# Kernel optimization log

Measured on AMD Instinct MI355X. Metric: run time of the kernel, lower is better.

The kernel has to match this reference:

```python
import jax, jax.numpy as jnp
import numpy as np

N = 100000
NFEAT = 128
NHID = 128
NCLASS = 40
E = 1600000
EPS = 1e-5


def _spmm(vals, src, dst, x, n):
    # y[dst] += vals * x[src]  (sparse adj @ x)
    return jax.ops.segment_sum(vals[:, None] * x[src], dst, num_segments=n)


def _bn(h, gamma, beta, rmean, rvar):
    # BatchNorm1d in eval mode (running statistics)
    return (h - rmean) * jax.lax.rsqrt(rvar + EPS) * gamma + beta


def setup_inputs() -> dict:
    key = jax.random.key(0)
    ks = jax.random.split(key, 24)
    inp = {
        'x': jax.random.normal(ks[0], (N, NFEAT), dtype=jnp.float32),
        'M': jax.random.uniform(ks[1], (N, 1), dtype=jnp.float32),
        'AM': jax.random.uniform(ks[2], (N, 1), dtype=jnp.float32),
        'srcZ': jax.random.randint(ks[3], (E,), 0, N, dtype=jnp.int32),
        'dstZ': jax.random.randint(ks[4], (E,), 0, N, dtype=jnp.int32),
        'valsZ': jax.random.uniform(ks[5], (E,), dtype=jnp.float32),
        'src': jax.random.randint(ks[6], (E,), 0, N, dtype=jnp.int32),
        'dst': jax.random.randint(ks[7], (E,), 0, N, dtype=jnp.int32),
        'vals': jax.random.uniform(ks[8], (E,), dtype=jnp.float32),
        # layer 0 (PaGConv) params
        'W0': jax.random.normal(ks[9], (NHID, NFEAT), dtype=jnp.float32) * (1.414 / np.sqrt(NFEAT)),
        'b0': jnp.zeros((NHID,), dtype=jnp.float32),
        'g0': jnp.ones((NHID,), dtype=jnp.float32),
        'be0': jnp.zeros((NHID,), dtype=jnp.float32),
        'rm0': jax.random.normal(ks[10], (NHID,), dtype=jnp.float32) * 0.1,
        'rv0': jax.random.uniform(ks[11], (NHID,), dtype=jnp.float32) + 0.5,
        # layer 1 (GConv) params
        'W1': jax.random.normal(ks[12], (NHID, NHID), dtype=jnp.float32) * (1.414 / np.sqrt(NHID)),
        'b1': jnp.zeros((NHID,), dtype=jnp.float32),
        'g1': jnp.ones((NHID,), dtype=jnp.float32),
        'be1': jnp.zeros((NHID,), dtype=jnp.float32),
        'rm1': jax.random.normal(ks[13], (NHID,), dtype=jnp.float32) * 0.1,
        'rv1': jax.random.uniform(ks[14], (NHID,), dtype=jnp.float32) + 0.5,
        # layer 2 (GConv) params
        'W2': jax.random.normal(ks[15], (NCLASS, NHID), dtype=jnp.float32) * (1.414 / np.sqrt(NHID)),
        'b2': jnp.zeros((NCLASS,), dtype=jnp.float32),
    }
    return inp


def reference(x, M, AM, srcZ, dstZ, valsZ, src, dst, vals,
              W0, b0, g0, be0, rm0, rv0,
              W1, b1, g1, be1, rm1, rv1,
              W2, b2):
    n = x.shape[0]
    # layer 0: PaGConv with adjZ: fc(spmm(adjZ, M*x) * AM), then BN + ReLU (dropout off in eval)
    h = _spmm(valsZ, srcZ, dstZ, M * x, n) * AM
    h = h @ W0.T + b0
    h = jax.nn.relu(_bn(h, g0, be0, rm0, rv0))
    # layer 1: GConv with adj: fc(spmm(adj, h)), then BN + ReLU
    h = _spmm(vals, src, dst, h, n)
    h = h @ W1.T + b1
    h = jax.nn.relu(_bn(h, g1, be1, rm1, rv1))
    # layer 2: GConv, then log_softmax
    h = _spmm(vals, src, dst, h, n)
    h = h @ W2.T + b2
    return jax.nn.log_softmax(h, axis=-1)
```

## Files before the change

kernel.cpp:

```cpp
#include <hip/hip_runtime.h>
#include <math.h>

#define NFEAT 128
#define NCLS 40
#define BINROWS 64
#define NBINMAX 1600
#define NBLKC 256
#define CHUNKMAX 6400
#define STHALF 3200
#define CEDGE 25
#define SEGC 7
#define RSMAX 2048

typedef short bf16x8 __attribute__((ext_vector_type(8)));
typedef float f32x4 __attribute__((ext_vector_type(4)));

__device__ __forceinline__ float bf2f(unsigned int lo16) {
  return __uint_as_float((lo16 & 0xffffu) << 16);
}
__device__ __forceinline__ unsigned int f2bf(float x) {
  unsigned int u = __float_as_uint(x);
  return (u + 0x7fffu + ((u >> 16) & 1u)) >> 16;
}

__device__ __forceinline__ int wave_incl_scan(int v, int lane64) {
  int s = v;
#pragma unroll
  for (int o = 1; o < 64; o <<= 1) {
    int x = __shfl_up(s, o);
    if (lane64 >= o) s += x;
  }
  return s;
}

__global__ __launch_bounds__(256) void sort_prep(
    const int* __restrict__ srcZ, const int* __restrict__ dstZ, const float* __restrict__ valZ,
    const int* __restrict__ srcA, const int* __restrict__ dstA, const float* __restrict__ valA,
    int2* __restrict__ DrmZ, int2* __restrict__ DrmA,
    int2* __restrict__ binsCZ, int2* __restrict__ binsCA,
    int E, int nbin, int chunk,
    const float* b0, const float* g0, const float* be0,
    const float* rm0, const float* rv0,
    const float* b1, const float* g1, const float* be1,
    const float* rm1, const float* rv1,
    float* sc0, float* sh0, float* sc1, float* sh1,
    const float* __restrict__ W0, const float* __restrict__ W1,
    const float* __restrict__ W2,
    unsigned short* __restrict__ Wb0, unsigned short* __restrict__ Wb1,
    unsigned short* __restrict__ W2hi, unsigned short* __restrict__ W2lo,
    const float* __restrict__ x, const float* __restrict__ Mv,
    unsigned short* __restrict__ xm, int n) {
  __shared__ int2 stage[STHALF];
  __shared__ int cur[NBINMAX];
  __shared__ int wsum[4];
  const int t = threadIdx.x;

  if (blockIdx.x >= 2 * NBLKC) {
    int pb = blockIdx.x - 2 * NBLKC;
    if (pb == 0) {
      if (t < 128) {
        float s = g0[t] * rsqrtf(rv0[t] + 1e-5f);
        sc0[t] = s;
        sh0[t] = (b0[t] - rm0[t]) * s + be0[t];
      } else {
        int i = t - 128;
        float s = g1[i] * rsqrtf(rv1[i] + 1e-5f);
        sc1[i] = s;
        sh1[i] = (b1[i] - rm1[i]) * s + be1[i];
      }
      return;
    }
    if (pb <= 20) {
      int i = (pb - 1) * 256 + t;
      if (i < 4096) {
        const float* W = (i < 2048) ? W0 : W1;
        unsigned short* Wb = (i < 2048) ? Wb0 : Wb1;
        int j = (i < 2048) ? i : i - 2048;
        const float4* p = (const float4*)(W + (size_t)j * 8);
        float4 v0 = p[0], v1 = p[1];
        unsigned int o0 = f2bf(v0.x) | (f2bf(v0.y) << 16);
        unsigned int o1 = f2bf(v0.z) | (f2bf(v0.w) << 16);
        unsigned int o2 = f2bf(v1.x) | (f2bf(v1.y) << 16);
        unsigned int o3 = f2bf(v1.z) | (f2bf(v1.w) << 16);
        ((uint4*)Wb)[j] = make_uint4(o0, o1, o2, o3);
      } else {
        int j = i - 4096;
        int r = j >> 4;
        float v[8] = {0.f, 0.f, 0.f, 0.f, 0.f, 0.f, 0.f, 0.f};
        if (r < NCLS) {
          const float4* p = (const float4*)(W2 + (size_t)j * 8);
          float4 a = p[0], b = p[1];
          v[0] = a.x; v[1] = a.y; v[2] = a.z; v[3] = a.w;
          v[4] = b.x; v[5] = b.y; v[6] = b.z; v[7] = b.w;
        }
        unsigned int h[8], l[8];
#pragma unroll
        for (int q = 0; q < 8; ++q) {
          h[q] = f2bf(v[q]);
          l[q] = f2bf(v[q] - bf2f(h[q]));
        }
        ((uint4*)W2hi)[j] = make_uint4(h[0] | (h[1] << 16), h[2] | (h[3] << 16),
                                       h[4] | (h[5] << 16), h[6] | (h[7] << 16));
        ((uint4*)W2lo)[j] = make_uint4(l[0] | (l[1] << 16), l[2] | (l[3] << 16),
                                       l[4] | (l[5] << 16), l[6] | (l[7] << 16));
      }
      return;
    }
    int i = (pb - 21) * 256 + t;
    if (i >= n * (NFEAT / 8)) return;
    int row = i >> 4;
    float m = Mv[row];
    const float4* p = (const float4*)(x + (size_t)i * 8);
    float4 v0 = p[0], v1 = p[1];
    unsigned int o0 = f2bf(v0.x * m) | (f2bf(v0.y * m) << 16);
    unsigned int o1 = f2bf(v0.z * m) | (f2bf(v0.w * m) << 16);
    unsigned int o2 = f2bf(v1.x * m) | (f2bf(v1.y * m) << 16);
    unsigned int o3 = f2bf(v1.z * m) | (f2bf(v1.w * m) << 16);
    ((uint4*)xm)[i] = make_uint4(o0, o1, o2, o3);
    return;
  }

  int k = blockIdx.x;
  const int* srcp; const int* dstp; const float* valp; int2* Drm; int2* binsC;
  if (k < NBLKC) {
    srcp = srcZ; dstp = dstZ; valp = valZ; Drm = DrmZ; binsC = binsCZ;
  } else {
    k -= NBLKC;
    srcp = srcA; dstp = dstA; valp = valA; Drm = DrmA; binsC = binsCA;
  }
  for (int i = t; i < nbin; i += 256) cur[i] = 0;
  __syncthreads();
  const int e0 = k * chunk, e1 = min(E, e0 + chunk);
  int pk[CEDGE];
#pragma unroll
  for (int j = 0; j < CEDGE; ++j) {
    int e = e0 + t + j * 256;
    if (e < e1) {
      int d = dstp[e];
      int bin = d >> 6;
      int r = atomicAdd(&cur[bin], 1);
      pk[j] = (bin << 19) | ((d & 63) << 13) | r;
    }
  }
  __syncthreads();
  int loc[SEGC], cnt[SEGC];
  int s = 0;
#pragma unroll
  for (int j = 0; j < SEGC; ++j) {
    int i = t * SEGC + j;
    int v = (i < nbin) ? cur[i] : 0;
    loc[j] = s; cnt[j] = v;
    s += v;
  }
  int incl = wave_incl_scan(s, t & 63);
  if ((t & 63) == 63) wsum[t >> 6] = incl;
  __syncthreads();
  int base = 0;
#pragma unroll
  for (int wv = 0; wv < 4; ++wv)
    if (wv < (t >> 6)) base += wsum[wv];
  int ex = base + incl - s;
#pragma unroll
  for (int j = 0; j < SEGC; ++j) {
    int i = t * SEGC + j;
    if (i < nbin) {
      int o = ex + loc[j];
      Drm[(size_t)k * nbin + i] = make_int2(e0 + o, cnt[j]);
      cur[i] = o;
    }
  }
  __syncthreads();
  const int nE = e1 - e0;
  const int hl = (nE + 1) >> 1;
#pragma unroll
  for (int j = 0; j < CEDGE; ++j) {
    int e = e0 + t + j * 256;
    if (e < e1) {
      int v = pk[j];
      int p = cur[(unsigned)v >> 19] + (v & 0x1FFF);
      if (p < hl)
        stage[p] = make_int2(srcp[e] | (((v >> 13) & 63) << 17), __float_as_int(valp[e]));
    }
  }
  __syncthreads();
  for (int i = t; i < hl; i += 256) binsC[e0 + i] = stage[i];
  __syncthreads();
#pragma unroll
  for (int j = 0; j < CEDGE; ++j) {
    int e = e0 + t + j * 256;
    if (e < e1) {
      int v = pk[j];
      int p = cur[(unsigned)v >> 19] + (v & 0x1FFF);
      if (p >= hl)
        stage[p - hl] = make_int2(srcp[e] | (((v >> 13) & 63) << 17), __float_as_int(valp[e]));
    }
  }
  __syncthreads();
  for (int i = t; i < nE - hl; i += 256) binsC[e0 + hl + i] = stage[i];
}

__global__ __launch_bounds__(256) void row_sort2(
    const int2* __restrict__ DrmZ, const int2* __restrict__ DrmA,
    const int2* __restrict__ binsCZ, const int2* __restrict__ binsCA,
    int2* __restrict__ bins2Z, int2* __restrict__ bins2A,
    int2* __restrict__ rdZ, int2* __restrict__ rdA, int n, int nbin) {
  __shared__ int2 stage[RSMAX];
  __shared__ short rankArr[RSMAX];
  __shared__ int wsum[4];
  __shared__ int rcnt[BINROWS];
  __shared__ int roff[BINROWS];
  const int nwg = 2 * nbin;
  const int q = nwg >> 3, r = nwg & 7;
  const int xcd = blockIdx.x & 7, idx = blockIdx.x >> 3;
  int b = (xcd < r ? xcd * (q + 1) : r * (q + 1) + (xcd - r) * q) + idx;
  const int t = threadIdx.x;
  const int2* Drm; const int2* binsC; int2* bins2; int2* rowdesc;
  if (b < nbin) {
    Drm = DrmZ; binsC = binsCZ; bins2 = bins2Z; rowdesc = rdZ;
  } else {
    b -= nbin;
    Drm = DrmA; binsC = binsCA; bins2 = bins2A; rowdesc = rdA;
  }
  if (t < BINROWS) rcnt[t] = 0;
  int2 run = Drm[(size_t)t * nbin + b];
  int incl = wave_incl_scan(run.y, t & 63);
  if ((t & 63) == 63) wsum[t >> 6] = incl;
  __syncthreads();
  int base = 0;
#pragma unroll
  for (int wv = 0; wv < 4; ++wv)
    if (wv < (t >> 6)) base += wsum[wv];
  int mystart = base + incl - run.y;
  int totalAll = wsum[0] + wsum[1] + wsum[2] + wsum[3];
  for (int j = 0; j < run.y; ++j) {
    int2 en = binsC[run.x + j];
    int idx2 = mystart + j;
    int rr = atomicAdd(&rcnt[(en.x >> 17) & 63], 1);
    if (idx2 < RSMAX) {
      stage[idx2] = en;
      rankArr[idx2] = (short)rr;
    }
  }
  __syncthreads();
  const int bs = b * RSMAX;
  if (t < BINROWS) {
    int c = rcnt[t];
    int s = c;
#pragma unroll
    for (int o = 1; o < 64; o <<= 1) {
      int v = __shfl_up(s, o);
      if (t >= o) s += v;
    }
    int excl = s - c;
    int row = b * BINROWS + t;
    if (row < n) rowdesc[row] = make_int2(bs + excl, c);
    roff[t] = excl;
  }
  __syncthreads();
  int total = min(totalAll, RSMAX);
  for (int i = t; i < total; i += 256) {
    int2 en = stage[i];
    int row = (en.x >> 17) & 63;
    bins2[bs + roff[row] + rankArr[i]] = en;
  }
}

template <bool SCALE>
__global__ __launch_bounds__(128) void spmm128_sorted(
    const int2* __restrict__ rowdesc, const int2* __restrict__ bins2,
    const unsigned short* __restrict__ X, const float* __restrict__ AM,
    unsigned short* __restrict__ Y, int n) {
  int row = (blockIdx.x * 128 + threadIdx.x) >> 6;
  int lane = threadIdx.x & 63;
  if (row >= n) return;
  int2 rd = rowdesc[row];
  int s = rd.x, d = rd.y;
  int half = lane >> 5, l32 = lane & 31;
  float s0 = 0.f, s1 = 0.f, s2 = 0.f, s3 = 0.f;
  for (int kb = 0; kb < d; kb += 64) {
    int rem = min(64, d - kb);
    int2 my = (lane < rem) ? bins2[s + kb + lane] : make_int2(0, 0);
    int myc = my.x & 0x1FFFF;
    float myw = __int_as_float(my.y);
    for (int k = 0; k < rem; k += 8) {
#pragma unroll
      for (int st = 0; st < 4; ++st) {
        int idx = k + 2 * st + half;
        int c = __shfl(myc, idx);
        float wv = __shfl(myw, idx);
        uint2 pv = *(const uint2*)(X + (size_t)c * NFEAT + l32 * 4);
        s0 += wv * bf2f(pv.x);
        s1 += wv * bf2f(pv.x >> 16);
        s2 += wv * bf2f(pv.y);
        s3 += wv * bf2f(pv.y >> 16);
      }
    }
  }
  s0 += __shfl_xor(s0, 32); s1 += __shfl_xor(s1, 32);
  s2 += __shfl_xor(s2, 32); s3 += __shfl_xor(s3, 32);
  if (SCALE) {
    float am = AM[row];
    s0 *= am; s1 *= am; s2 *= am; s3 *= am;
  }
  unsigned int pk = half ? (f2bf(s2) | (f2bf(s3) << 16)) : (f2bf(s0) | (f2bf(s1) << 16));
  ((unsigned int*)Y)[(size_t)row * (NFEAT / 2) + l32 * 2 + half] = pk;
}

template <bool FUSE_G2>
__global__ __launch_bounds__(256) void gemm_mfma128(
    const unsigned short* __restrict__ Y, const unsigned short* __restrict__ Wb,
    const float* __restrict__ scale, const float* __restrict__ shift,
    unsigned short* __restrict__ Out,
    const unsigned short* __restrict__ Whi, const unsigned short* __restrict__ Wlo,
    unsigned short* __restrict__ G2, int M) {
  const int wave = threadIdx.x >> 6;
  const int lane = threadIdx.x & 63;
  const int quad = lane >> 4;
  const int l16 = lane & 15;
  const int arow = blockIdx.x * 64 + wave * 16 + l16;
  const bool rv = arow < M;

  f32x4 acc[8];
#pragma unroll
  for (int c = 0; c < 8; ++c) acc[c] = (f32x4){0.f, 0.f, 0.f, 0.f};

#pragma unroll
  for (int kc = 0; kc < 128; kc += 32) {
    bf16x8 a = rv ? *(const bf16x8*)(Y + (size_t)arow * 128 + kc + quad * 8)
                  : (bf16x8){0, 0, 0, 0, 0, 0, 0, 0};
#pragma unroll
    for (int c = 0; c < 8; ++c) {
      bf16x8 b = *(const bf16x8*)(Wb + (size_t)(c * 16 + l16) * 128 + kc + quad * 8);
      acc[c] = __builtin_amdgcn_mfma_f32_16x16x32_bf16(a, b, acc[c], 0, 0, 0);
    }
  }

  const int orow0 = blockIdx.x * 64 + wave * 16 + quad * 4;

  if constexpr (!FUSE_G2) {
#pragma unroll
    for (int c = 0; c < 8; ++c) {
      int col = c * 16 + l16;
      float sc = scale[col], sh = shift[col];
#pragma unroll
      for (int r = 0; r < 4; ++r) {
        int orow = orow0 + r;
        if (orow < M) {
          float v = fmaxf(acc[c][r] * sc + sh, 0.f);
          Out[(size_t)orow * 128 + col] = (unsigned short)f2bf(v);
        }
      }
    }
  } else {
    __shared__ unsigned short Ht[64][136];
    const int lrow0 = wave * 16 + quad * 4;
#pragma unroll
    for (int c = 0; c < 8; ++c) {
      int col = c * 16 + l16;
      float sc = scale[col], sh = shift[col];
#pragma unroll
      for (int r = 0; r < 4; ++r) {
        float v = fmaxf(acc[c][r] * sc + sh, 0.f);
        Ht[lrow0 + r][col] = (unsigned short)f2bf(v);
      }
    }
    __syncthreads();
    bf16x8 af[4];
#pragma unroll
    for (int kc = 0; kc < 4; ++kc)
      af[kc] = *(const bf16x8*)(&Ht[wave * 16 + l16][kc * 32 + quad * 8]);
    f32x4 acc2[3];
#pragma unroll
    for (int c2 = 0; c2 < 3; ++c2) acc2[c2] = (f32x4){0.f, 0.f, 0.f, 0.f};
#pragma unroll
    for (int kc = 0; kc < 4; ++kc) {
#pragma unroll
      for (int c2 = 0; c2 < 3; ++c2) {
        bf16x8 bh = *(const bf16x8*)(Whi + (size_t)(c2 * 16 + l16) * 128 + kc * 32 + quad * 8);
        bf16x8 bl = *(const bf16x8*)(Wlo + (size_t)(c2 * 16 + l16) * 128 + kc * 32 + quad * 8);
        acc2[c2] = __builtin_amdgcn_mfma_f32_16x16x32_bf16(af[kc], bh, acc2[c2], 0, 0, 0);
        acc2[c2] = __builtin_amdgcn_mfma_f32_16x16x32_bf16(af[kc], bl, acc2[c2], 0, 0, 0);
      }
    }
#pragma unroll
    for (int c2 = 0; c2 < 3; ++c2) {
      int col = c2 * 16 + l16;
      if (col < NCLS) {
#pragma unroll
        for (int r = 0; r < 4; ++r) {
          int orow = orow0 + r;
          if (orow < M) G2[(size_t)orow * NCLS + col] = (unsigned short)f2bf(acc2[c2][r]);
        }
      }
    }
  }
}

__global__ __launch_bounds__(128) void spmm_softmax64(
    const int2* __restrict__ rowdesc, const int2* __restrict__ bins2,
    const unsigned short* __restrict__ G2, const float* __restrict__ b2,
    float* __restrict__ out, int n) {
  int row = (blockIdx.x * 128 + threadIdx.x) >> 6;
  int lane = threadIdx.x & 63;
  if (row >= n) return;
  const int eidx = lane >> 4, q = lane & 15;
  const bool vq = q < (NCLS / 4);
  float4 bv = vq ? *(const float4*)(b2 + q * 4) : make_float4(0.f, 0.f, 0.f, 0.f);

  int2 rdv = rowdesc[row];
  int s0i = rdv.x, d = rdv.y;
  float a0 = 0.f, a1 = 0.f, a2 = 0.f, a3 = 0.f;
  for (int kb = 0; kb < d; kb += 64) {
    int rem = min(64, d - kb);
    int2 my = (lane < rem) ? bins2[s0i + kb + lane] : make_int2(0, 0);
    int myc = my.x & 0x1FFFF;
    float myw = __int_as_float(my.y);
    int steps = (rem + 3) >> 2;
#pragma unroll 4
    for (int st = 0; st < steps; ++st) {
      int idx = st * 4 + eidx;
      int c = __shfl(myc, idx);
      float wv = __shfl(myw, idx);
      if (vq) {
        uint2 pv = *(const uint2*)(G2 + (size_t)c * NCLS + q * 4);
        a0 += wv * bf2f(pv.x);
        a1 += wv * bf2f(pv.x >> 16);
        a2 += wv * bf2f(pv.y);
        a3 += wv * bf2f(pv.y >> 16);
      }
    }
  }
  a0 += __shfl_xor(a0, 16); a1 += __shfl_xor(a1, 16);
  a2 += __shfl_xor(a2, 16); a3 += __shfl_xor(a3, 16);
  a0 += __shfl_xor(a0, 32); a1 += __shfl_xor(a1, 32);
  a2 += __shfl_xor(a2, 32); a3 += __shfl_xor(a3, 32);
  float z0 = a0 + bv.x, z1 = a1 + bv.y, z2 = a2 + bv.z, z3 = a3 + bv.w;
  bool par = (eidx == 0) && vq;
  float m = par ? fmaxf(fmaxf(z0, z1), fmaxf(z2, z3)) : -INFINITY;
#pragma unroll
  for (int o = 1; o < 64; o <<= 1) m = fmaxf(m, __shfl_xor(m, o));
  float ex = par ? (__expf(z0 - m) + __expf(z1 - m) + __expf(z2 - m) + __expf(z3 - m)) : 0.f;
#pragma unroll
  for (int o = 1; o < 64; o <<= 1) ex += __shfl_xor(ex, o);
  float lg = m + __logf(ex);
  if (par) {
    *(float4*)&out[(size_t)row * NCLS + q * 4] =
        make_float4(z0 - lg, z1 - lg, z2 - lg, z3 - lg);
  }
}


extern "C" void kernel_launch(void* const* d_in, const int* in_sizes, int n_in,
                              void* d_out, int out_size, void* d_ws, size_t ws_size,
                              hipStream_t stream) {
  const float* x    = (const float*)d_in[0];
  const float* Mv   = (const float*)d_in[1];
  const float* AM   = (const float*)d_in[2];
  const int* srcZ   = (const int*)d_in[3];
  const int* dstZ   = (const int*)d_in[4];
  const float* valsZ= (const float*)d_in[5];
  const int* src    = (const int*)d_in[6];
  const int* dst    = (const int*)d_in[7];
  const float* vals = (const float*)d_in[8];
  const float* W0   = (const float*)d_in[9];
  const float* b0   = (const float*)d_in[10];
  const float* g0   = (const float*)d_in[11];
  const float* be0  = (const float*)d_in[12];
  const float* rm0  = (const float*)d_in[13];
  const float* rv0  = (const float*)d_in[14];
  const float* W1   = (const float*)d_in[15];
  const float* b1   = (const float*)d_in[16];
  const float* g1   = (const float*)d_in[17];
  const float* be1  = (const float*)d_in[18];
  const float* rm1  = (const float*)d_in[19];
  const float* rv1  = (const float*)d_in[20];
  const float* W2   = (const float*)d_in[21];
  const float* b2   = (const float*)d_in[22];
  float* out = (float*)d_out;

  const int N = in_sizes[1];
  const int E = in_sizes[3];
  const int NBIN = (N + BINROWS - 1) / BINROWS;
  const int CHUNK = (E + NBLKC - 1) / NBLKC;

  char* w = (char*)d_ws;
  size_t off = 0;
  auto alloc = [&](size_t bytes) -> void* {
    void* p = w + off;
    off = (off + bytes + 255) & ~(size_t)255;
    return p;
  };
  const size_t bins2Bytes = (size_t)NBIN * RSMAX * 8;
  const size_t bufBytes = (size_t)N * NFEAT * 2;
  int2* binsCZ = (int2*)alloc((size_t)NBLKC * CHUNK * 8);
  int2* binsCA = (int2*)alloc((size_t)NBLKC * CHUNK * 8);
  int2* bins2A = (int2*)alloc(bins2Bytes);
  int2* rdZ = (int2*)alloc((size_t)N * 8);
  int2* rdA = (int2*)alloc((size_t)N * 8);
  unsigned short* xm = (unsigned short*)alloc(bufBytes);
  unsigned short* bufA = (unsigned short*)alloc(bufBytes);
  unsigned short* bufB = (unsigned short*)alloc(bins2Bytes > bufBytes ? bins2Bytes : bufBytes);
  float* sc0 = (float*)alloc(128 * 4);
  float* sh0 = (float*)alloc(128 * 4);
  float* sc1 = (float*)alloc(128 * 4);
  float* sh1 = (float*)alloc(128 * 4);
  unsigned short* Wb0 = (unsigned short*)alloc(128 * 128 * 2);
  unsigned short* Wb1 = (unsigned short*)alloc(128 * 128 * 2);
  unsigned short* W2hi = (unsigned short*)alloc(64 * 128 * 2);
  unsigned short* W2lo = (unsigned short*)alloc(64 * 128 * 2);
  const size_t drmBytes = (size_t)NBLKC * NBIN * 8;
  int2* DrmZ = (int2*)((char*)bufA + 0 * drmBytes);
  int2* DrmA = (int2*)((char*)bufA + 1 * drmBytes);
  int2* bins2Z = (int2*)bufB;
  unsigned short* G2 = bufB;

  const int RB2 = (N + 1) / 2;
  const int GB64 = (N + 63) / 64;
  const int CONVB = (N * (NFEAT / 8) + 255) / 256;

  sort_prep<<<2 * NBLKC + 21 + CONVB, 256, 0, stream>>>(
      srcZ, dstZ, valsZ, src, dst, vals, DrmZ, DrmA, binsCZ, binsCA, E, NBIN, CHUNK,
      b0, g0, be0, rm0, rv0, b1, g1, be1, rm1, rv1, sc0, sh0, sc1, sh1,
      W0, W1, W2, Wb0, Wb1, W2hi, W2lo, x, Mv, xm, N);

  row_sort2<<<2 * NBIN, 256, 0, stream>>>(DrmZ, DrmA, binsCZ, binsCA,
                                          bins2Z, bins2A, rdZ, rdA, N, NBIN);

  spmm128_sorted<true><<<RB2, 128, 0, stream>>>(rdZ, bins2Z, xm, AM, bufA, N);
  gemm_mfma128<false><<<GB64, 256, 0, stream>>>(bufA, Wb0, sc0, sh0, bufB,
                                                nullptr, nullptr, nullptr, N);

  spmm128_sorted<false><<<RB2, 128, 0, stream>>>(rdA, bins2A, bufB,
                                                 (const float*)nullptr, bufA, N);
  gemm_mfma128<true><<<GB64, 256, 0, stream>>>(bufA, Wb1, sc1, sh1, nullptr,
                                               W2hi, W2lo, G2, N);

  spmm_softmax64<<<RB2, 128, 0, stream>>>(rdA, bins2A, G2, b2, out, N);
}
```

Measured before the change: 480.9 us.

## Overlap adjacency row-sort with layer-0 SpMM in a single fused launch

Splits the combined row-sort kernel so the Z adjacency is sorted first. The A adjacency sort then runs in the same launch as the layer-0 SpMM, with blocks dispatched by block index. This lets the independent A sort overlap with the memory-bound SpMM and removes one launch boundary. The Drm buffers move out of bufA into their own workspace, because bufA is now written by the SpMM while the A sort still reads DrmA. The fused kernel uses 256-thread blocks carrying the larger LDS footprint of the sort for the SpMM blocks too, which may lower SpMM occupancy.

```diff
diff --git a/kernel.cpp b/kernel.cpp
--- a/kernel.cpp
+++ b/kernel.cpp
@@ -31,6 +31,12 @@
     if (lane64 >= o) s += x;
   }
   return s;
+}
+
+__device__ __forceinline__ int xcd_swizzle(int bid, int nwg) {
+  const int q = nwg >> 3, r = nwg & 7;
+  const int xcd = bid & 7, idx = bid >> 3;
+  return (xcd < r ? xcd * (q + 1) : r * (q + 1) + (xcd - r) * q) + idx;
 }
 
 __global__ __launch_bounds__(256) void sort_prep(
@@ -199,28 +205,16 @@
   for (int i = t; i < nE - hl; i += 256) binsC[e0 + hl + i] = stage[i];
 }
 
-__global__ __launch_bounds__(256) void row_sort2(
-    const int2* __restrict__ DrmZ, const int2* __restrict__ DrmA,
-    const int2* __restrict__ binsCZ, const int2* __restrict__ binsCA,
-    int2* __restrict__ bins2Z, int2* __restrict__ bins2A,
-    int2* __restrict__ rdZ, int2* __restrict__ rdA, int n, int nbin) {
+__device__ __forceinline__ void row_sort_body(
+    const int2* __restrict__ Drm, const int2* __restrict__ binsC,
+    int2* __restrict__ bins2, int2* __restrict__ rowdesc,
+    int n, int nbin, int b) {
   __shared__ int2 stage[RSMAX];
   __shared__ short rankArr[RSMAX];
   __shared__ int wsum[4];
   __shared__ int rcnt[BINROWS];
   __shared__ int roff[BINROWS];
-  const int nwg = 2 * nbin;
-  const int q = nwg >> 3, r = nwg & 7;
-  const int xcd = blockIdx.x & 7, idx = blockIdx.x >> 3;
-  int b = (xcd < r ? xcd * (q + 1) : r * (q + 1) + (xcd - r) * q) + idx;
   const int t = threadIdx.x;
-  const int2* Drm; const int2* binsC; int2* bins2; int2* rowdesc;
-  if (b < nbin) {
-    Drm = DrmZ; binsC = binsCZ; bins2 = bins2Z; rowdesc = rdZ;
-  } else {
-    b -= nbin;
-    Drm = DrmA; binsC = binsCA; bins2 = bins2A; rowdesc = rdA;
-  }
   if (t < BINROWS) rcnt[t] = 0;
   int2 run = Drm[(size_t)t * nbin + b];
   int incl = wave_incl_scan(run.y, t & 63);
@@ -265,13 +259,18 @@
   }
 }
 
+__global__ __launch_bounds__(256) void row_sortZ_k(
+    const int2* __restrict__ DrmZ, const int2* __restrict__ binsCZ,
+    int2* __restrict__ bins2Z, int2* __restrict__ rdZ, int n, int nbin) {
+  int b = xcd_swizzle(blockIdx.x, nbin);
+  row_sort_body(DrmZ, binsCZ, bins2Z, rdZ, n, nbin, b);
+}
+
 template <bool SCALE>
-__global__ __launch_bounds__(128) void spmm128_sorted(
+__device__ __forceinline__ void spmm_row_body(
     const int2* __restrict__ rowdesc, const int2* __restrict__ bins2,
     const unsigned short* __restrict__ X, const float* __restrict__ AM,
-    unsigned short* __restrict__ Y, int n) {
-  int row = (blockIdx.x * 128 + threadIdx.x) >> 6;
-  int lane = threadIdx.x & 63;
+    unsigned short* __restrict__ Y, int n, int row, int lane) {
   if (row >= n) return;
   int2 rd = rowdesc[row];
   int s = rd.x, d = rd.y;
@@ -304,6 +303,30 @@
   }
   unsigned int pk = half ? (f2bf(s2) | (f2bf(s3) << 16)) : (f2bf(s0) | (f2bf(s1) << 16));
   ((unsigned int*)Y)[(size_t)row * (NFEAT / 2) + l32 * 2 + half] = pk;
+}
+
+template <bool SCALE>
+__global__ __launch_bounds__(128) void spmm128_sorted(
+    const int2* __restrict__ rowdesc, const int2* __restrict__ bins2,
+    const unsigned short* __restrict__ X, const float* __restrict__ AM,
+    unsigned short* __restrict__ Y, int n) {
+  int row = (blockIdx.x * 128 + threadIdx.x) >> 6;
+  spmm_row_body<SCALE>(rowdesc, bins2, X, AM, Y, n, row, threadIdx.x & 63);
+}
+
+__global__ __launch_bounds__(256) void rsA_spmmZ(
+    const int2* __restrict__ DrmA, const int2* __restrict__ binsCA,
+    int2* __restrict__ bins2A, int2* __restrict__ rdA,
+    const int2* __restrict__ rdZ, const int2* __restrict__ bins2Z,
+    const unsigned short* __restrict__ xm, const float* __restrict__ AM,
+    unsigned short* __restrict__ Y0, int n, int nbin) {
+  if ((int)blockIdx.x < nbin) {
+    int b = xcd_swizzle(blockIdx.x, nbin);
+    row_sort_body(DrmA, binsCA, bins2A, rdA, n, nbin, b);
+  } else {
+    int row = ((int)blockIdx.x - nbin) * 4 + (threadIdx.x >> 6);
+    spmm_row_body<true>(rdZ, bins2Z, xm, AM, Y0, n, row, threadIdx.x & 63);
+  }
 }
 
 template <bool FUSE_G2>
@@ -494,6 +517,8 @@
   const size_t bufBytes = (size_t)N * NFEAT * 2;
   int2* binsCZ = (int2*)alloc((size_t)NBLKC * CHUNK * 8);
   int2* binsCA = (int2*)alloc((size_t)NBLKC * CHUNK * 8);
+  int2* DrmZ = (int2*)alloc((size_t)NBLKC * NBIN * 8);
+  int2* DrmA = (int2*)alloc((size_t)NBLKC * NBIN * 8);
   int2* bins2A = (int2*)alloc(bins2Bytes);
   int2* rdZ = (int2*)alloc((size_t)N * 8);
   int2* rdA = (int2*)alloc((size_t)N * 8);
@@ -508,13 +533,11 @@
   unsigned short* Wb1 = (unsigned short*)alloc(128 * 128 * 2);
   unsigned short* W2hi = (unsigned short*)alloc(64 * 128 * 2);
   unsigned short* W2lo = (unsigned short*)alloc(64 * 128 * 2);
-  const size_t drmBytes = (size_t)NBLKC * NBIN * 8;
-  int2* DrmZ = (int2*)((char*)bufA + 0 * drmBytes);
-  int2* DrmA = (int2*)((char*)bufA + 1 * drmBytes);
   int2* bins2Z = (int2*)bufB;
   unsigned short* G2 = bufB;
 
   const int RB2 = (N + 1) / 2;
+  const int RB4 = (N + 3) / 4;
   const int GB64 = (N + 63) / 64;
   const int CONVB = (N * (NFEAT / 8) + 255) / 256;
 
@@ -523,10 +546,11 @@
       b0, g0, be0, rm0, rv0, b1, g1, be1, rm1, rv1, sc0, sh0, sc1, sh1,
       W0, W1, W2, Wb0, Wb1, W2hi, W2lo, x, Mv, xm, N);
 
-  row_sort2<<<2 * NBIN, 256, 0, stream>>>(DrmZ, DrmA, binsCZ, binsCA,
-                                          bins2Z, bins2A, rdZ, rdA, N, NBIN);
-
-  spmm128_sorted<true><<<RB2, 128, 0, stream>>>(rdZ, bins2Z, xm, AM, bufA, N);
+  row_sortZ_k<<<NBIN, 256, 0, stream>>>(DrmZ, binsCZ, bins2Z, rdZ, N, NBIN);
+
+  rsA_spmmZ<<<NBIN + RB4, 256, 0, stream>>>(DrmA, binsCA, bins2A, rdA,
+                                            rdZ, bins2Z, xm, AM, bufA, N, NBIN);
+
   gemm_mfma128<false><<<GB64, 256, 0, stream>>>(bufA, Wb0, sc0, sh0, bufB,
                                                 nullptr, nullptr, nullptr, N);
 
```

Result: no change. 482.7 us (+0.4%).
